# Kernel optimization log

Hardware: AMD Instinct MI355X
Metric: run time of the kernel (lower is better)

Reference implementation:

```python
import jax, jax.numpy as jnp
import numpy as np

EPS = 1e-3  # keras LayerNormalization default epsilon

def setup_inputs() -> dict:
    key = jax.random.key(0)
    k1, k2 = jax.random.split(key)
    B, N, D, M = 16, 4096, 768, 8
    x = jax.random.normal(k1, (B, N, D), dtype=jnp.float32)
    queries = jax.random.normal(k2, (M, D), dtype=jnp.float32)
    gamma = jnp.ones((D,), dtype=jnp.float32)
    beta = jnp.zeros((D,), dtype=jnp.float32)
    return {"x": x, "queries": queries, "gamma": gamma, "beta": beta}

def reference(x, queries, gamma, beta):
    D = x.shape[-1]
    scale = D ** -0.5
    # LayerNorm over last dim (keras default: epsilon=1e-3, learned gamma/beta)
    mu = jnp.mean(x, axis=-1, keepdims=True)
    var = jnp.mean(jnp.square(x - mu), axis=-1, keepdims=True)
    xn = (x - mu) * jax.lax.rsqrt(var + EPS) * gamma + beta  # [B, N, D]
    # sim = queries @ (x^T * scale) -> [B, M, N]
    sim = jnp.einsum('md,bnd->bmn', queries, xn) * scale
    attn = jax.nn.softmax(sim, axis=-1)
    # out = attn @ x_normed -> [B, M, D]
    return jnp.einsum('bmn,bnd->bmd', attn, xn)
```

## Files before the change

kernel.cpp:

```cpp
#include <hip/hip_runtime.h>
#include <hip/hip_bf16.h>


#define B_ 16
#define N_ 4096
#define D_ 768
#define M_ 8
#define EPS_ 1e-3f
#define SCALE_ 0.03608439182435161f

#define SIM_OFF   0
#define MEAN_OFF  524288
#define RSTD_OFF  589824
#define SMAX_OFF  655360
#define SINV_OFF  655488

__global__ __launch_bounds__(256) void k_ln_sim(
    const float* __restrict__ x,
    const float* __restrict__ q,
    const float* __restrict__ gm,
    const float* __restrict__ bt,
    float* __restrict__ sim, float* __restrict__ meanb, float* __restrict__ rstdb)
{
    const int lane = threadIdx.x & 63;
    const int gw   = blockIdx.x * 4 + (threadIdx.x >> 6);
    const int total_waves = gridDim.x * 4;

    float g[12], bb[12], qr[8][12];
#pragma unroll
    for (int i = 0; i < 3; i++) {
        const int c4 = (lane + i * 64) * 4;
        float4 gv = *(const float4*)(gm + c4);
        float4 bv = *(const float4*)(bt + c4);
        g[i * 4 + 0] = gv.x; g[i * 4 + 1] = gv.y; g[i * 4 + 2] = gv.z; g[i * 4 + 3] = gv.w;
        bb[i * 4 + 0] = bv.x; bb[i * 4 + 1] = bv.y; bb[i * 4 + 2] = bv.z; bb[i * 4 + 3] = bv.w;
#pragma unroll
        for (int m = 0; m < 8; m++) {
            float4 qv = *(const float4*)(q + m * D_ + c4);
            qr[m][i * 4 + 0] = qv.x; qr[m][i * 4 + 1] = qv.y;
            qr[m][i * 4 + 2] = qv.z; qr[m][i * 4 + 3] = qv.w;
        }
    }

    for (int row = gw; row < B_ * N_; row += total_waves) {
        const float* xr = x + (size_t)row * D_;
        float v[12];
#pragma unroll
        for (int i = 0; i < 3; i++) {
            float4 p = *(const float4*)(xr + (lane + i * 64) * 4);
            v[i * 4 + 0] = p.x; v[i * 4 + 1] = p.y;
            v[i * 4 + 2] = p.z; v[i * 4 + 3] = p.w;
        }
        float s = 0.f, s2 = 0.f;
#pragma unroll
        for (int k = 0; k < 12; k++) { s += v[k]; s2 += v[k] * v[k]; }
#pragma unroll
        for (int mask = 32; mask; mask >>= 1) {
            s  += __shfl_xor(s,  mask, 64);
            s2 += __shfl_xor(s2, mask, 64);
        }
        const float mean = s * (1.0f / 768.0f);
        float var = s2 * (1.0f / 768.0f) - mean * mean;
        var = fmaxf(var, 0.0f);
        const float rstd = rsqrtf(var + EPS_);

        float acc[8];
#pragma unroll
        for (int m = 0; m < 8; m++) acc[m] = 0.f;
#pragma unroll
        for (int k = 0; k < 12; k++) {
            const float xn = (v[k] - mean) * rstd * g[k] + bb[k];
#pragma unroll
            for (int m = 0; m < 8; m++) acc[m] = fmaf(qr[m][k], xn, acc[m]);
        }
#pragma unroll
        for (int mask = 32; mask; mask >>= 1)
#pragma unroll
            for (int m = 0; m < 8; m++) acc[m] += __shfl_xor(acc[m], mask, 64);

        if (lane == 0) {
            const int b = row >> 12, n = row & (N_ - 1);
            meanb[row] = mean;
            rstdb[row] = rstd;
#pragma unroll
            for (int m = 0; m < 8; m++)
                sim[(size_t)((b * 8 + m) << 12) + n] = acc[m] * SCALE_;
        }
    }
}

__global__ __launch_bounds__(256) void k_stats(
    const float* __restrict__ sim, float* __restrict__ smax, float* __restrict__ sinv)
{
    const float* p = sim + (size_t)blockIdx.x * N_;
    const int t = threadIdx.x;
    const int lane = t & 63, wave = t >> 6;
    __shared__ float red[4];

    float v[16];
    float mx = -3.4e38f;
#pragma unroll
    for (int i = 0; i < 16; i++) { v[i] = p[t + i * 256]; mx = fmaxf(mx, v[i]); }
#pragma unroll
    for (int mask = 32; mask; mask >>= 1) mx = fmaxf(mx, __shfl_xor(mx, mask, 64));
    if (lane == 0) red[wave] = mx;
    __syncthreads();
    mx = fmaxf(fmaxf(red[0], red[1]), fmaxf(red[2], red[3]));
    __syncthreads();

    float s = 0.f;
#pragma unroll
    for (int i = 0; i < 16; i++) s += __expf(v[i] - mx);
#pragma unroll
    for (int mask = 32; mask; mask >>= 1) s += __shfl_xor(s, mask, 64);
    if (lane == 0) red[wave] = s;
    __syncthreads();
    if (t == 0) {
        s = red[0] + red[1] + red[2] + red[3];
        smax[blockIdx.x] = mx;
        sinv[blockIdx.x] = 1.0f / s;
    }
}

__global__ __launch_bounds__(256) void k_out(
    const float* __restrict__ x,
    const float* __restrict__ gm,
    const float* __restrict__ bt,
    const float* __restrict__ sim,
    const float* __restrict__ meanb,
    const float* __restrict__ rstdb,
    const float* __restrict__ smax,
    const float* __restrict__ sinv,
    float* __restrict__ out)
{
    __shared__ float w_s[8 * 64];
    __shared__ float mean_s[64];
    __shared__ float rstd_s[64];

    const int b = blockIdx.x >> 6;
    const int n0 = (blockIdx.x & 63) * 64;
    const int t = threadIdx.x;

#pragma unroll
    for (int k = 0; k < 2; k++) {
        const int idx = t + k * 256;
        const int m = idx >> 6, nn = idx & 63;
        const float v = sim[(size_t)((b * 8 + m) << 12) + n0 + nn];
        w_s[idx] = __expf(v - smax[b * 8 + m]) * sinv[b * 8 + m];
    }
    if (t < 64) {
        mean_s[t] = meanb[b * N_ + n0 + t];
        rstd_s[t] = rstdb[b * N_ + n0 + t];
    }
    __syncthreads();

    const float g0 = gm[t],       bb0 = bt[t];
    const float g1 = gm[t + 256], bb1 = bt[t + 256];
    const float g2 = gm[t + 512], bb2 = bt[t + 512];

    float acc[8][3];
#pragma unroll
    for (int m = 0; m < 8; m++)
#pragma unroll
        for (int j = 0; j < 3; j++) acc[m][j] = 0.f;

    const float* xb = x + ((size_t)(b * N_ + n0)) * D_;
#pragma unroll 4
    for (int nn = 0; nn < 64; nn++) {
        const float* xr = xb + (size_t)nn * D_;
        const float mu = mean_s[nn], rs = rstd_s[nn];
        const float xn0 = (xr[t]       - mu) * rs * g0 + bb0;
        const float xn1 = (xr[t + 256] - mu) * rs * g1 + bb1;
        const float xn2 = (xr[t + 512] - mu) * rs * g2 + bb2;
#pragma unroll
        for (int m = 0; m < 8; m++) {
            const float a = w_s[m * 64 + nn];
            acc[m][0] = fmaf(a, xn0, acc[m][0]);
            acc[m][1] = fmaf(a, xn1, acc[m][1]);
            acc[m][2] = fmaf(a, xn2, acc[m][2]);
        }
    }

#pragma unroll
    for (int mm = 0; mm < 8; mm++) {
        const int m = (mm + (blockIdx.x & 7)) & 7;
        float* o = out + (size_t)(b * 8 + m) * D_;
        atomicAdd(o + t,       acc[m][0]);
        atomicAdd(o + t + 256, acc[m][1]);
        atomicAdd(o + t + 512, acc[m][2]);
    }
}

extern "C" void kernel_launch(void* const* d_in, const int* in_sizes, int n_in,
                              void* d_out, int out_size, void* d_ws, size_t ws_size,
                              hipStream_t stream)
{
    const float* x  = (const float*)d_in[0];
    const float* q  = (const float*)d_in[1];
    const float* gm = (const float*)d_in[2];
    const float* bt = (const float*)d_in[3];
    float* out = (float*)d_out;

    float* ws    = (float*)d_ws;
    float* sim   = ws + SIM_OFF;
    float* meanb = ws + MEAN_OFF;
    float* rstdb = ws + RSTD_OFF;
    float* smax  = ws + SMAX_OFF;
    float* sinv  = ws + SINV_OFF;

    hipMemsetAsync(out, 0, (size_t)B_ * M_ * D_ * sizeof(float), stream);

    k_ln_sim<<<2048, 256, 0, stream>>>(x, q, gm, bt, sim, meanb, rstdb);
    k_stats<<<B_ * M_, 256, 0, stream>>>(sim, smax, sinv);
    k_out<<<B_ * 64, 256, 0, stream>>>(x, gm, bt, sim, meanb, rstdb, smax, sinv, out);
}
```

Before: 333.1 us.

## Use butterfly multi-reduce in LN-sim, fold memset into stats, float4 out kernel

New measurement: 392.2 us. 1.18x slower.

```diff
diff --git a/kernel.cpp b/kernel.cpp
--- a/kernel.cpp
+++ b/kernel.cpp
@@ -42,6 +42,10 @@
         }
     }
 
+    const bool hi32 = (lane & 32) != 0;
+    const bool hi16 = (lane & 16) != 0;
+    const bool hi8  = (lane & 8)  != 0;
+
     for (int row = gw; row < B_ * N_; row += total_waves) {
         const float* xr = x + (size_t)row * D_;
         float v[12];
@@ -73,30 +77,49 @@
 #pragma unroll
             for (int m = 0; m < 8; m++) acc[m] = fmaf(qr[m][k], xn, acc[m]);
         }
-#pragma unroll
-        for (int mask = 32; mask; mask >>= 1)
-#pragma unroll
-            for (int m = 0; m < 8; m++) acc[m] += __shfl_xor(acc[m], mask, 64);
-
+
+        float a0 = hi32 ? acc[4] : acc[0], sA0 = hi32 ? acc[0] : acc[4];
+        float a1 = hi32 ? acc[5] : acc[1], sA1 = hi32 ? acc[1] : acc[5];
+        float a2 = hi32 ? acc[6] : acc[2], sA2 = hi32 ? acc[2] : acc[6];
+        float a3 = hi32 ? acc[7] : acc[3], sA3 = hi32 ? acc[3] : acc[7];
+        a0 += __shfl_xor(sA0, 32, 64);
+        a1 += __shfl_xor(sA1, 32, 64);
+        a2 += __shfl_xor(sA2, 32, 64);
+        a3 += __shfl_xor(sA3, 32, 64);
+        float b0 = hi16 ? a2 : a0, sB0 = hi16 ? a0 : a2;
+        float b1 = hi16 ? a3 : a1, sB1 = hi16 ? a1 : a3;
+        b0 += __shfl_xor(sB0, 16, 64);
+        b1 += __shfl_xor(sB1, 16, 64);
+        float c0 = hi8 ? b1 : b0, sC0 = hi8 ? b0 : b1;
+        c0 += __shfl_xor(sC0, 8, 64);
+        c0 += __shfl_xor(c0, 4, 64);
+        c0 += __shfl_xor(c0, 2, 64);
+        c0 += __shfl_xor(c0, 1, 64);
+
+        const int b = row >> 12, n = row & (N_ - 1);
         if (lane == 0) {
-            const int b = row >> 12, n = row & (N_ - 1);
             meanb[row] = mean;
             rstdb[row] = rstd;
-#pragma unroll
-            for (int m = 0; m < 8; m++)
-                sim[(size_t)((b * 8 + m) << 12) + n] = acc[m] * SCALE_;
+        }
+        if ((lane & 7) == 0) {
+            const int m = lane >> 3;
+            sim[(size_t)((b * 8 + m) << 12) + n] = c0 * SCALE_;
         }
     }
 }
 
 __global__ __launch_bounds__(256) void k_stats(
-    const float* __restrict__ sim, float* __restrict__ smax, float* __restrict__ sinv)
+    const float* __restrict__ sim, float* __restrict__ smax, float* __restrict__ sinv,
+    float* __restrict__ out0)
 {
     const float* p = sim + (size_t)blockIdx.x * N_;
     const int t = threadIdx.x;
     const int lane = t & 63, wave = t >> 6;
     __shared__ float red[4];
 
+    const int gid = blockIdx.x * 256 + t;
+    out0[gid] = 0.f; out0[gid + 32768] = 0.f; out0[gid + 65536] = 0.f;
+
     float v[16];
     float mx = -3.4e38f;
 #pragma unroll
@@ -122,7 +145,7 @@
     }
 }
 
-__global__ __launch_bounds__(256) void k_out(
+__global__ __launch_bounds__(192) void k_out(
     const float* __restrict__ x,
     const float* __restrict__ gm,
     const float* __restrict__ bt,
@@ -141,9 +164,7 @@
     const int n0 = (blockIdx.x & 63) * 64;
     const int t = threadIdx.x;
 
-#pragma unroll
-    for (int k = 0; k < 2; k++) {
-        const int idx = t + k * 256;
+    for (int idx = t; idx < 8 * 64; idx += 192) {
         const int m = idx >> 6, nn = idx & 63;
         const float v = sim[(size_t)((b * 8 + m) << 12) + n0 + nn];
         w_s[idx] = __expf(v - smax[b * 8 + m]) * sinv[b * 8 + m];
@@ -154,40 +175,43 @@
     }
     __syncthreads();
 
-    const float g0 = gm[t],       bb0 = bt[t];
-    const float g1 = gm[t + 256], bb1 = bt[t + 256];
-    const float g2 = gm[t + 512], bb2 = bt[t + 512];
-
-    float acc[8][3];
+    const int c4 = t * 4;
+    const float4 g4 = *(const float4*)(gm + c4);
+    const float4 b4 = *(const float4*)(bt + c4);
+
+    float acc[8][4];
 #pragma unroll
     for (int m = 0; m < 8; m++)
 #pragma unroll
-        for (int j = 0; j < 3; j++) acc[m][j] = 0.f;
+        for (int j = 0; j < 4; j++) acc[m][j] = 0.f;
 
     const float* xb = x + ((size_t)(b * N_ + n0)) * D_;
-#pragma unroll 4
+#pragma unroll 2
     for (int nn = 0; nn < 64; nn++) {
-        const float* xr = xb + (size_t)nn * D_;
+        const float4 xv = *(const float4*)(xb + (size_t)nn * D_ + c4);
         const float mu = mean_s[nn], rs = rstd_s[nn];
-        const float xn0 = (xr[t]       - mu) * rs * g0 + bb0;
-        const float xn1 = (xr[t + 256] - mu) * rs * g1 + bb1;
-        const float xn2 = (xr[t + 512] - mu) * rs * g2 + bb2;
+        const float xn0 = (xv.x - mu) * rs * g4.x + b4.x;
+        const float xn1 = (xv.y - mu) * rs * g4.y + b4.y;
+        const float xn2 = (xv.z - mu) * rs * g4.z + b4.z;
+        const float xn3 = (xv.w - mu) * rs * g4.w + b4.w;
 #pragma unroll
         for (int m = 0; m < 8; m++) {
             const float a = w_s[m * 64 + nn];
             acc[m][0] = fmaf(a, xn0, acc[m][0]);
             acc[m][1] = fmaf(a, xn1, acc[m][1]);
             acc[m][2] = fmaf(a, xn2, acc[m][2]);
+            acc[m][3] = fmaf(a, xn3, acc[m][3]);
         }
     }
 
 #pragma unroll
     for (int mm = 0; mm < 8; mm++) {
         const int m = (mm + (blockIdx.x & 7)) & 7;
-        float* o = out + (size_t)(b * 8 + m) * D_;
-        atomicAdd(o + t,       acc[m][0]);
-        atomicAdd(o + t + 256, acc[m][1]);
-        atomicAdd(o + t + 512, acc[m][2]);
+        float* o = out + (size_t)(b * 8 + m) * D_ + c4;
+        atomicAdd(o + 0, acc[m][0]);
+        atomicAdd(o + 1, acc[m][1]);
+        atomicAdd(o + 2, acc[m][2]);
+        atomicAdd(o + 3, acc[m][3]);
     }
 }
 
@@ -208,9 +232,7 @@
     float* smax  = ws + SMAX_OFF;
     float* sinv  = ws + SINV_OFF;
 
-    hipMemsetAsync(out, 0, (size_t)B_ * M_ * D_ * sizeof(float), stream);
-
     k_ln_sim<<<2048, 256, 0, stream>>>(x, q, gm, bt, sim, meanb, rstdb);
-    k_stats<<<B_ * M_, 256, 0, stream>>>(sim, smax, sinv);
-    k_out<<<B_ * 64, 256, 0, stream>>>(x, gm, bt, sim, meanb, rstdb, smax, sinv, out);
-}
+    k_stats<<<B_ * M_, 256, 0, stream>>>(sim, smax, sinv, out);
+    k_out<<<B_ * 64, 192, 0, stream>>>(x, gm, bt, sim, meanb, rstdb, smax, sinv, out);
+}
```

## Fold LayerNorm into query projection, transpose-reduce sims, fuse output zeroing

Applied to the files above, without the earlier changes.

New measurement: 329.4 us. About the same (-1.1%).

```diff
diff --git a/kernel.cpp b/kernel.cpp
--- a/kernel.cpp
+++ b/kernel.cpp
@@ -26,21 +26,44 @@
     const int gw   = blockIdx.x * 4 + (threadIdx.x >> 6);
     const int total_waves = gridDim.x * 4;
 
-    float g[12], bb[12], qr[8][12];
+    float qg[8][12];
+    float qgs[8], qb[8];
+#pragma unroll
+    for (int m = 0; m < 8; m++) { qgs[m] = 0.f; qb[m] = 0.f; }
 #pragma unroll
     for (int i = 0; i < 3; i++) {
         const int c4 = (lane + i * 64) * 4;
         float4 gv = *(const float4*)(gm + c4);
         float4 bv = *(const float4*)(bt + c4);
-        g[i * 4 + 0] = gv.x; g[i * 4 + 1] = gv.y; g[i * 4 + 2] = gv.z; g[i * 4 + 3] = gv.w;
-        bb[i * 4 + 0] = bv.x; bb[i * 4 + 1] = bv.y; bb[i * 4 + 2] = bv.z; bb[i * 4 + 3] = bv.w;
 #pragma unroll
         for (int m = 0; m < 8; m++) {
             float4 qv = *(const float4*)(q + m * D_ + c4);
-            qr[m][i * 4 + 0] = qv.x; qr[m][i * 4 + 1] = qv.y;
-            qr[m][i * 4 + 2] = qv.z; qr[m][i * 4 + 3] = qv.w;
-        }
-    }
+            qg[m][i * 4 + 0] = qv.x * gv.x;
+            qg[m][i * 4 + 1] = qv.y * gv.y;
+            qg[m][i * 4 + 2] = qv.z * gv.z;
+            qg[m][i * 4 + 3] = qv.w * gv.w;
+            qgs[m] += qg[m][i * 4 + 0] + qg[m][i * 4 + 1] + qg[m][i * 4 + 2] + qg[m][i * 4 + 3];
+            qb[m]  += qv.x * bv.x + qv.y * bv.y + qv.z * bv.z + qv.w * bv.w;
+        }
+    }
+#pragma unroll
+    for (int mask = 32; mask; mask >>= 1)
+#pragma unroll
+        for (int m = 0; m < 8; m++) {
+            qgs[m] += __shfl_xor(qgs[m], mask, 64);
+            qb[m]  += __shfl_xor(qb[m],  mask, 64);
+        }
+    const int mo = lane >> 3;
+    const float qgs_sel =
+        (mo & 4) ? ((mo & 2) ? ((mo & 1) ? qgs[7] : qgs[6]) : ((mo & 1) ? qgs[5] : qgs[4]))
+                 : ((mo & 2) ? ((mo & 1) ? qgs[3] : qgs[2]) : ((mo & 1) ? qgs[1] : qgs[0]));
+    const float qbs = SCALE_ *
+        ((mo & 4) ? ((mo & 2) ? ((mo & 1) ? qb[7] : qb[6]) : ((mo & 1) ? qb[5] : qb[4]))
+                  : ((mo & 2) ? ((mo & 1) ? qb[3] : qb[2]) : ((mo & 1) ? qb[1] : qb[0])));
+
+    const bool hi32 = (lane & 32) != 0;
+    const bool hi16 = (lane & 16) != 0;
+    const bool hi8  = (lane & 8)  != 0;
 
     for (int row = gw; row < B_ * N_; row += total_waves) {
         const float* xr = x + (size_t)row * D_;
@@ -54,6 +77,14 @@
         float s = 0.f, s2 = 0.f;
 #pragma unroll
         for (int k = 0; k < 12; k++) { s += v[k]; s2 += v[k] * v[k]; }
+        float acc[8];
+#pragma unroll
+        for (int m = 0; m < 8; m++) acc[m] = 0.f;
+#pragma unroll
+        for (int k = 0; k < 12; k++)
+#pragma unroll
+            for (int m = 0; m < 8; m++) acc[m] = fmaf(qg[m][k], v[k], acc[m]);
+
 #pragma unroll
         for (int mask = 32; mask; mask >>= 1) {
             s  += __shfl_xor(s,  mask, 64);
@@ -64,38 +95,47 @@
         var = fmaxf(var, 0.0f);
         const float rstd = rsqrtf(var + EPS_);
 
-        float acc[8];
-#pragma unroll
-        for (int m = 0; m < 8; m++) acc[m] = 0.f;
-#pragma unroll
-        for (int k = 0; k < 12; k++) {
-            const float xn = (v[k] - mean) * rstd * g[k] + bb[k];
-#pragma unroll
-            for (int m = 0; m < 8; m++) acc[m] = fmaf(qr[m][k], xn, acc[m]);
-        }
-#pragma unroll
-        for (int mask = 32; mask; mask >>= 1)
-#pragma unroll
-            for (int m = 0; m < 8; m++) acc[m] += __shfl_xor(acc[m], mask, 64);
-
+        float a0 = hi32 ? acc[4] : acc[0], sA0 = hi32 ? acc[0] : acc[4];
+        float a1 = hi32 ? acc[5] : acc[1], sA1 = hi32 ? acc[1] : acc[5];
+        float a2 = hi32 ? acc[6] : acc[2], sA2 = hi32 ? acc[2] : acc[6];
+        float a3 = hi32 ? acc[7] : acc[3], sA3 = hi32 ? acc[3] : acc[7];
+        a0 += __shfl_xor(sA0, 32, 64);
+        a1 += __shfl_xor(sA1, 32, 64);
+        a2 += __shfl_xor(sA2, 32, 64);
+        a3 += __shfl_xor(sA3, 32, 64);
+        float b0 = hi16 ? a2 : a0, sB0 = hi16 ? a0 : a2;
+        float b1 = hi16 ? a3 : a1, sB1 = hi16 ? a1 : a3;
+        b0 += __shfl_xor(sB0, 16, 64);
+        b1 += __shfl_xor(sB1, 16, 64);
+        float c0 = hi8 ? b1 : b0, sC0 = hi8 ? b0 : b1;
+        c0 += __shfl_xor(sC0, 8, 64);
+        c0 += __shfl_xor(c0, 4, 64);
+        c0 += __shfl_xor(c0, 2, 64);
+        c0 += __shfl_xor(c0, 1, 64);
+
+        const int b = row >> 12, n = row & (N_ - 1);
         if (lane == 0) {
-            const int b = row >> 12, n = row & (N_ - 1);
             meanb[row] = mean;
             rstdb[row] = rstd;
-#pragma unroll
-            for (int m = 0; m < 8; m++)
-                sim[(size_t)((b * 8 + m) << 12) + n] = acc[m] * SCALE_;
+        }
+        if ((lane & 7) == 0) {
+            sim[(size_t)((b * 8 + mo) << 12) + n] =
+                fmaf(rstd * SCALE_, c0 - mean * qgs_sel, qbs);
         }
     }
 }
 
 __global__ __launch_bounds__(256) void k_stats(
-    const float* __restrict__ sim, float* __restrict__ smax, float* __restrict__ sinv)
+    const float* __restrict__ sim, float* __restrict__ smax, float* __restrict__ sinv,
+    float* __restrict__ out0)
 {
     const float* p = sim + (size_t)blockIdx.x * N_;
     const int t = threadIdx.x;
     const int lane = t & 63, wave = t >> 6;
     __shared__ float red[4];
+
+    const int gid = blockIdx.x * 256 + t;
+    out0[gid] = 0.f; out0[gid + 32768] = 0.f; out0[gid + 65536] = 0.f;
 
     float v[16];
     float mx = -3.4e38f;
@@ -208,9 +248,7 @@
     float* smax  = ws + SMAX_OFF;
     float* sinv  = ws + SINV_OFF;
 
-    hipMemsetAsync(out, 0, (size_t)B_ * M_ * D_ * sizeof(float), stream);
-
     k_ln_sim<<<2048, 256, 0, stream>>>(x, q, gm, bt, sim, meanb, rstdb);
-    k_stats<<<B_ * M_, 256, 0, stream>>>(sim, smax, sinv);
+    k_stats<<<B_ * M_, 256, 0, stream>>>(sim, smax, sinv, out);
     k_out<<<B_ * 64, 256, 0, stream>>>(x, gm, bt, sim, meanb, rstdb, smax, sinv, out);
 }
```
